# Kernel optimization log

Measured on AMD Instinct MI355X. Metric: run time of the kernel, lower is better.

Reference implementation:

```python
import jax, jax.numpy as jnp
import numpy as np

P = 21            # patch_size
DP = 2            # dilation_patch
PAD = DP * (P // 2)  # 20
EPS = 1e-5


def setup_inputs() -> dict:
    key = jax.random.key(0)
    k1, k2 = jax.random.split(key)
    B, T_total, C, H, W = 4, 8, 64, 64, 64
    out_channels = 64
    feats_ts = jax.random.normal(k1, (B, T_total, C, H, W), dtype=jnp.float32)
    bn_gamma = jnp.ones((P * P,), dtype=jnp.float32)
    bn_beta = jnp.zeros((P * P,), dtype=jnp.float32)
    conv_w = jax.random.normal(k2, (out_channels, P * P), dtype=jnp.float32) * 0.05
    return {"feats_ts": feats_ts, "bn_gamma": bn_gamma, "bn_beta": bn_beta, "conv_w": conv_w}


def _correlation(f1, f2):
    # f1, f2: [N, C, H, W]. SpatialCorrelationSampler with kernel=1, stride=1,
    # pad=0, dilation=1, dilation_patch=2: out[n, p, q, h, w] =
    #   sum_c f1[n, c, h, w] * f2[n, c, h + 2*(p - P//2), w + 2*(q - P//2)]
    N, C, H, W = f1.shape
    padded = jnp.pad(f2, ((0, 0), (0, 0), (PAD, PAD), (PAD, PAD)))
    offs = jnp.arange(P) * DP              # displacement offsets into padded map
    dy = jnp.repeat(offs, P)               # [P*P]
    dx = jnp.tile(offs, P)                 # [P*P]

    def corr_at(oy, ox):
        shifted = jax.lax.dynamic_slice(padded, (0, 0, oy, ox), (N, C, H, W))
        return jnp.einsum('nchw,nchw->nhw', f1, shifted)  # sum over channels

    cor = jax.vmap(corr_at)(dy, dx)        # [P*P, N, H, W]
    return jnp.transpose(cor, (1, 0, 2, 3))  # [N, P*P, H, W]


def reference(feats_ts, bn_gamma, bn_beta, conv_w):
    B, T_total, C, H, W = feats_ts.shape
    T = T_total - 1
    f1 = feats_ts[:, :-1].reshape(B * T, C, H, W)
    f2 = feats_ts[:, 1:].reshape(B * T, C, H, W)

    cor = _correlation(f1, f2)             # [B*T, P*P, H, W]

    # BatchNorm2d (training mode: batch statistics over N, H, W)
    mean = cor.mean(axis=(0, 2, 3))
    var = cor.var(axis=(0, 2, 3))
    xn = (cor - mean[None, :, None, None]) * jax.lax.rsqrt(var + EPS)[None, :, None, None]
    xn = xn * bn_gamma[None, :, None, None] + bn_beta[None, :, None, None]

    # 1x1 conv, no bias: [B*T, out, H, W]
    out = jnp.einsum('nphw,op->nohw', xn, conv_w)
    out = out.reshape(B, T, out.shape[1], H, W)
    # append zero frame along time: [B, T+1, out, H, W]
    out = jnp.concatenate([out, jnp.zeros_like(out[:, :1])], axis=1)
    return out
```

## Files before the change

kernel.cpp:

```cpp
#include <hip/hip_runtime.h>

#define HW   4096
#define CHW  262144
#define NPQ  441
#define KPAD 448
#define CSTR 456
#define CSTA 460

typedef __attribute__((ext_vector_type(8))) short bf16x8;
typedef __attribute__((ext_vector_type(4))) float f32x4;

#define MFMA16(a,b,c) __builtin_amdgcn_mfma_f32_16x16x32_bf16(a,b,c,0,0,0)

__device__ __forceinline__ short f2bf(float f){
  unsigned u = __float_as_uint(f);
  return (short)((u + 0x7FFFu + ((u >> 16) & 1u)) >> 16);
}
__device__ __forceinline__ float bf2f(short s){
  return __uint_as_float(((unsigned)(unsigned short)s) << 16);
}

__device__ __forceinline__ bf16x8 load_fragX(const short* rowX, int pi, int tile,
                                             int kk, int lane){
  const int m = lane & 15, kg = lane >> 4;
  return *(const bf16x8*)(rowX + (2*(tile*16 + m) + pi)*64 + kk*32 + kg*8);
}

__global__ __launch_bounds__(256,4) void k_transpose(const float* __restrict__ feats,
                                                     short* __restrict__ X, int plane0)
{
  __shared__ float tile[64*65];
  const int tid = threadIdx.x;
  const int pll = blockIdx.x >> 6, h = blockIdx.x & 63;
  const float* pb = feats + (size_t)(plane0 + pll)*CHW + h*64;
#pragma unroll
  for (int k = 0; k < 4; ++k){
    const int idx = tid + k*256;
    const int c = idx >> 4, w4 = idx & 15;
    f32x4 v = *(const f32x4*)(pb + c*HW + w4*4);
#pragma unroll
    for (int j = 0; j < 4; ++j) tile[c*65 + w4*4 + j] = v[j];
  }
  __syncthreads();
  short* xb = X + ((size_t)pll*64 + h)*4096;
#pragma unroll
  for (int s = 0; s < 2; ++s){
    const int chunk = tid + s*256;
    const int w = chunk >> 3, cg = chunk & 7;
    bf16x8 r;
#pragma unroll
    for (int j = 0; j < 8; ++j) r[j] = f2bf(tile[(cg*8 + j)*65 + w]);
    *(bf16x8*)(xb + w*64 + cg*8) = r;
  }
}

__global__ __launch_bounds__(256,4) void k_cor2(const short* __restrict__ X,
    short* __restrict__ corg, float* __restrict__ partS, float* __restrict__ partQ)
{
  __shared__ __align__(16) short tile[32*CSTA];
  const int tid = threadIdx.x, wv = tid >> 6, lane = tid & 63;
  const int bi = blockIdx.x;
  const int pi = bi & 1, h = (bi >> 1) & 63, nn = bi >> 7;
  const int pl1 = (nn/7)*8 + (nn%7);
  const short* f1r  = X + ((size_t)pl1*64 + h)*4096;
  const short* f2pl = X + (size_t)(pl1 + 1)*64*4096;

  {
    int4 z = {0,0,0,0};
    for (int idx = tid; idx < 32*CSTA/8; idx += 256) ((int4*)tile)[idx] = z;
  }

  bf16x8 afr[2][2];
#pragma unroll
  for (int mt = 0; mt < 2; ++mt)
#pragma unroll
    for (int kk = 0; kk < 2; ++kk)
      afr[mt][kk] = load_fragX(f1r, pi, mt, kk, lane);

  __syncthreads();

  const int cI = (lane >> 4)*4;
  const int cJ = lane & 15;

  auto clampr = [&](int r){ return r < 0 ? 0 : (r > 63 ? 63 : r); };
  bf16x8 b[4], nb[4];
  {
    const int row0 = clampr(h + 2*wv - 20);
    const short* f2r = f2pl + row0*4096;
    b[0] = load_fragX(f2r, pi, 0, 0, lane);
    b[1] = load_fragX(f2r, pi, 1, 0, lane);
    b[2] = load_fragX(f2r, pi, 0, 1, lane);
    b[3] = load_fragX(f2r, pi, 1, 1, lane);
  }
  for (int it = 0; it < 6; ++it){
    const int u = it*4 + wv;
    const int row = h + 2*u - 20;
    if (it < 5){
      const int rown = clampr(row + 8);
      const short* f2r = f2pl + rown*4096;
      nb[0] = load_fragX(f2r, pi, 0, 0, lane);
      nb[1] = load_fragX(f2r, pi, 1, 0, lane);
      nb[2] = load_fragX(f2r, pi, 0, 1, lane);
      nb[3] = load_fragX(f2r, pi, 1, 1, lane);
    }
    if (u < 21 && (unsigned)row < 64u){
      f32x4 a00 = {0.f,0.f,0.f,0.f}, a01 = a00, a10 = a00, a11 = a00;
      a00 = MFMA16(afr[0][0], b[0], a00);
      a01 = MFMA16(afr[0][0], b[1], a01);
      a10 = MFMA16(afr[1][0], b[0], a10);
      a11 = MFMA16(afr[1][0], b[1], a11);
      a00 = MFMA16(afr[0][1], b[2], a00);
      a01 = MFMA16(afr[0][1], b[3], a01);
      a10 = MFMA16(afr[1][1], b[2], a10);
      a11 = MFMA16(afr[1][1], b[3], a11);
      const int p21 = u*21;
#define SCAT(v, ii, jj) do{ int q_ = (jj) - (ii) + 10; \
        if ((unsigned)q_ < 21u) tile[(ii)*CSTA + p21 + q_] = f2bf(v); }while(0)
#pragma unroll
      for (int r = 0; r < 4; ++r){
        const int i0 = cI + r;
        SCAT(a00[r], i0,      cJ);
        SCAT(a01[r], i0,      cJ + 16);
        SCAT(a10[r], i0 + 16, cJ);
        SCAT(a11[r], i0 + 16, cJ + 16);
      }
#undef SCAT
    }
#pragma unroll
    for (int j = 0; j < 4; ++j) b[j] = nb[j];
  }
  __syncthreads();

  {
    const int g = tid >> 2, sub = tid & 3;
    if (g < 56){
      float s[8], s2[8];
#pragma unroll
      for (int j = 0; j < 8; ++j){ s[j] = 0.f; s2[j] = 0.f; }
      for (int rr = 0; rr < 8; ++rr){
        const int row = sub*8 + rr;
        bf16x8 v = *(const bf16x8*)&tile[row*CSTA + g*8];
#pragma unroll
        for (int j = 0; j < 8; ++j){
          float f = bf2f(v[j]);
          s[j] += f; s2[j] += f*f;
        }
      }
#pragma unroll
      for (int j = 0; j < 8; ++j){
        s[j]  += __shfl_xor(s[j], 1);  s[j]  += __shfl_xor(s[j], 2);
        s2[j] += __shfl_xor(s2[j], 1); s2[j] += __shfl_xor(s2[j], 2);
      }
      if (sub == 0){
        float* ps = partS + (size_t)bi*KPAD + g*8;
        float* pq = partQ + (size_t)bi*KPAD + g*8;
        *(f32x4*)ps       = (f32x4){s[0], s[1], s[2], s[3]};
        *(f32x4*)(ps + 4) = (f32x4){s[4], s[5], s[6], s[7]};
        *(f32x4*)pq       = (f32x4){s2[0], s2[1], s2[2], s2[3]};
        *(f32x4*)(pq + 4) = (f32x4){s2[4], s2[5], s2[6], s2[7]};
      }
    }
  }

  short* cblk = corg + (size_t)bi*14336;
  for (int c = tid; c < 1792; c += 256){
    const int row = c/56, cg = c - row*56;
    *(bf16x8*)(cblk + row*KPAD + cg*8) = *(const bf16x8*)&tile[row*CSTA + cg*8];
  }
}

__global__ __launch_bounds__(256) void k_red2(const float* __restrict__ partS,
    const float* __restrict__ partQ, const float* __restrict__ gamma,
    const float* __restrict__ beta, float* __restrict__ scalek,
    float* __restrict__ shiftk)
{
  __shared__ float redS[4][8], redQ[4][8];
  const int tid = threadIdx.x, wv = tid >> 6, lane = tid & 63;
  const int g = blockIdx.x;
  float s[8], q[8];
#pragma unroll
  for (int j = 0; j < 8; ++j){ s[j] = 0.f; q[j] = 0.f; }
  for (int it = 0; it < 14; ++it){
    const int slot = tid + it*256;
    const float* ps = partS + (size_t)slot*KPAD + g*8;
    const float* pq = partQ + (size_t)slot*KPAD + g*8;
    f32x4 a0 = *(const f32x4*)ps, a1 = *(const f32x4*)(ps + 4);
    f32x4 b0 = *(const f32x4*)pq, b1 = *(const f32x4*)(pq + 4);
#pragma unroll
    for (int j = 0; j < 4; ++j){
      s[j] += a0[j]; s[j+4] += a1[j];
      q[j] += b0[j]; q[j+4] += b1[j];
    }
  }
#pragma unroll
  for (int off = 1; off < 64; off <<= 1){
#pragma unroll
    for (int j = 0; j < 8; ++j){
      s[j] += __shfl_xor(s[j], off);
      q[j] += __shfl_xor(q[j], off);
    }
  }
  if (lane == 0){
#pragma unroll
    for (int j = 0; j < 8; ++j){ redS[wv][j] = s[j]; redQ[wv][j] = q[j]; }
  }
  __syncthreads();
  if (tid < 8){
    const int k = g*8 + tid;
    float st = redS[0][tid] + redS[1][tid] + redS[2][tid] + redS[3][tid];
    float qt = redQ[0][tid] + redQ[1][tid] + redQ[2][tid] + redQ[3][tid];
    float m  = st * (1.f/114688.f);
    float v  = qt * (1.f/114688.f) - m*m;
    float iv = rsqrtf(v + 1e-5f);
    float gm = (k < NPQ) ? gamma[k] : 0.f;
    float bt = (k < NPQ) ? beta[k]  : 0.f;
    float sc = gm * iv;
    scalek[k] = sc;
    shiftk[k] = bt - m*sc;
  }
}

__global__ __launch_bounds__(256) void k_wfold(const float* __restrict__ scalek,
    const float* __restrict__ shiftk, const float* __restrict__ convw,
    short* __restrict__ wpT, float* __restrict__ bias)
{
  __shared__ float red[4];
  const int o = blockIdx.x, tid = threadIdx.x, wv = tid >> 6, lane = tid & 63;
  float part = 0.f;
#pragma unroll
  for (int s = 0; s < 2; ++s){
    const int k = tid + s*256;
    if (k < KPAD){
      float cw = (k < NPQ) ? convw[o*NPQ + k] : 0.f;
      wpT[o*KPAD + k] = f2bf(cw * scalek[k]);
      part += cw * shiftk[k];
    }
  }
#pragma unroll
  for (int off = 1; off < 64; off <<= 1) part += __shfl_xor(part, off);
  if (lane == 0) red[wv] = part;
  __syncthreads();
  if (tid == 0) bias[o] = red[0] + red[1] + red[2] + red[3];
}

__global__ __launch_bounds__(256,2) void k_main2(const short* __restrict__ corg,
    const short* __restrict__ wpT, const float* __restrict__ bias,
    float* __restrict__ out)
{
  __shared__ __align__(16) short cor[64*CSTR];
  const int tid = threadIdx.x, wv = tid >> 6, lane = tid & 63;
  const int nn = blockIdx.x >> 6, h = blockIdx.x & 63;
  const int pl1g = (nn/7)*8 + (nn%7);
  const short* cblk = corg + (size_t)(nn*64 + h)*28672;

#pragma unroll
  for (int s = 0; s < 14; ++s){
    const int c = tid + s*256;
    const int rho = c/56, cg = c - rho*56;
    const int w = ((rho & 31) << 1) | (rho >> 5);
    bf16x8 v = *(const bf16x8*)(cblk + c*8);
    *(bf16x8*)&cor[w*CSTR + cg*8] = v;
  }
  __syncthreads();

  const int m = lane & 15, kg = lane >> 4;
  const short* wrow = wpT + (wv*16 + m)*KPAD;
  f32x4 acc[4];
#pragma unroll
  for (int nt = 0; nt < 4; ++nt) acc[nt] = (f32x4){0.f,0.f,0.f,0.f};
  for (int kk = 0; kk < 14; ++kk){
    const int k0 = kk*32 + kg*8;
    bf16x8 aw = *(const bf16x8*)(wrow + k0);
#pragma unroll
    for (int nt = 0; nt < 4; ++nt){
      bf16x8 bc = *(const bf16x8*)&cor[(nt*16 + m)*CSTR + k0];
      acc[nt] = MFMA16(aw, bc, acc[nt]);
    }
  }
  const int r0 = (lane >> 4)*4;
  float bo[4];
#pragma unroll
  for (int r = 0; r < 4; ++r) bo[r] = bias[wv*16 + r0 + r];
  float* outb = out + (size_t)pl1g*CHW + h*64;
#pragma unroll
  for (int nt = 0; nt < 4; ++nt)
#pragma unroll
    for (int r = 0; r < 4; ++r){
      const int o = wv*16 + r0 + r;
      outb[o*HW + nt*16 + m] = acc[nt][r] + bo[r];
    }
}

__global__ __launch_bounds__(256,4) void k_cor(const short* __restrict__ X,
    short* __restrict__ corg, float* __restrict__ gpartS, float* __restrict__ gpartQ)
{
  __shared__ __align__(16) short tile[32*CSTA];
  const int tid = threadIdx.x, wv = tid >> 6, lane = tid & 63;
  const int bi = blockIdx.x;
  const int pi = bi & 1, h = (bi >> 1) & 63, nn = bi >> 7;
  const int pl1 = (nn/7)*8 + (nn%7);
  const short* f1r  = X + ((size_t)pl1*64 + h)*4096;
  const short* f2pl = X + (size_t)(pl1 + 1)*64*4096;

  {
    int4 z = {0,0,0,0};
    for (int idx = tid; idx < 32*CSTA/8; idx += 256) ((int4*)tile)[idx] = z;
  }
  bf16x8 afr[2][2];
#pragma unroll
  for (int mt = 0; mt < 2; ++mt)
#pragma unroll
    for (int kk = 0; kk < 2; ++kk)
      afr[mt][kk] = load_fragX(f1r, pi, mt, kk, lane);
  __syncthreads();
  const int cI = (lane >> 4)*4;
  const int cJ = lane & 15;
  auto clampr = [&](int r){ return r < 0 ? 0 : (r > 63 ? 63 : r); };
  bf16x8 b[4], nb[4];
  {
    const int row0 = clampr(h + 2*wv - 20);
    const short* f2r = f2pl + row0*4096;
    b[0] = load_fragX(f2r, pi, 0, 0, lane);
    b[1] = load_fragX(f2r, pi, 1, 0, lane);
    b[2] = load_fragX(f2r, pi, 0, 1, lane);
    b[3] = load_fragX(f2r, pi, 1, 1, lane);
  }
  for (int it = 0; it < 6; ++it){
    const int u = it*4 + wv;
    const int row = h + 2*u - 20;
    if (it < 5){
      const int rown = clampr(row + 8);
      const short* f2r = f2pl + rown*4096;
      nb[0] = load_fragX(f2r, pi, 0, 0, lane);
      nb[1] = load_fragX(f2r, pi, 1, 0, lane);
      nb[2] = load_fragX(f2r, pi, 0, 1, lane);
      nb[3] = load_fragX(f2r, pi, 1, 1, lane);
    }
    if (u < 21 && (unsigned)row < 64u){
      f32x4 a00 = {0.f,0.f,0.f,0.f}, a01 = a00, a10 = a00, a11 = a00;
      a00 = MFMA16(afr[0][0], b[0], a00);
      a01 = MFMA16(afr[0][0], b[1], a01);
      a10 = MFMA16(afr[1][0], b[0], a10);
      a11 = MFMA16(afr[1][0], b[1], a11);
      a00 = MFMA16(afr[0][1], b[2], a00);
      a01 = MFMA16(afr[0][1], b[3], a01);
      a10 = MFMA16(afr[1][1], b[2], a10);
      a11 = MFMA16(afr[1][1], b[3], a11);
      const int p21 = u*21;
#define SCAT(v, ii, jj) do{ int q_ = (jj) - (ii) + 10; \
        if ((unsigned)q_ < 21u) tile[(ii)*CSTA + p21 + q_] = f2bf(v); }while(0)
#pragma unroll
      for (int r = 0; r < 4; ++r){
        const int i0 = cI + r;
        SCAT(a00[r], i0,      cJ);
        SCAT(a01[r], i0,      cJ + 16);
        SCAT(a10[r], i0 + 16, cJ);
        SCAT(a11[r], i0 + 16, cJ + 16);
      }
#undef SCAT
    }
#pragma unroll
    for (int j = 0; j < 4; ++j) b[j] = nb[j];
  }
  __syncthreads();
  {
    const int g = tid >> 2, sub = tid & 3;
    if (g < 56){
      float s[8], s2[8];
#pragma unroll
      for (int j = 0; j < 8; ++j){ s[j] = 0.f; s2[j] = 0.f; }
      for (int rr = 0; rr < 8; ++rr){
        const int row = sub*8 + rr;
        bf16x8 v = *(const bf16x8*)&tile[row*CSTA + g*8];
#pragma unroll
        for (int j = 0; j < 8; ++j){
          float f = bf2f(v[j]);
          s[j] += f; s2[j] += f*f;
        }
      }
#pragma unroll
      for (int j = 0; j < 8; ++j){
        s[j]  += __shfl_xor(s[j], 1);  s[j]  += __shfl_xor(s[j], 2);
        s2[j] += __shfl_xor(s2[j], 1); s2[j] += __shfl_xor(s2[j], 2);
      }
      if (sub == 0){
        const int slot = (bi & 31)*KPAD + g*8;
#pragma unroll
        for (int j = 0; j < 8; ++j){
          atomicAdd(&gpartS[slot + j], s[j]);
          atomicAdd(&gpartQ[slot + j], s2[j]);
        }
      }
    }
  }
  short* cblk = corg + (size_t)bi*14336;
  for (int c = tid; c < 1792; c += 256){
    const int row = c/56, cg = c - row*56;
    *(bf16x8*)(cblk + row*KPAD + cg*8) = *(const bf16x8*)&tile[row*CSTA + cg*8];
  }
}

__global__ __launch_bounds__(256) void k_finalizeB(const float* __restrict__ gpartS,
    const float* __restrict__ gpartQ, const float* __restrict__ gamma,
    const float* __restrict__ beta, const float* __restrict__ convw,
    short* __restrict__ wpT, float* __restrict__ bias)
{
  __shared__ float s_scale[NPQ], s_shift[NPQ];
  const int tid = threadIdx.x;
  for (int k = tid; k < NPQ; k += 256){
    float s = 0.f, q = 0.f;
    for (int sl = 0; sl < 32; ++sl){
      s += gpartS[sl*KPAD + k];
      q += gpartQ[sl*KPAD + k];
    }
    float m  = s * (1.f/114688.f);
    float v  = q * (1.f/114688.f) - m*m;
    float iv = rsqrtf(v + 1e-5f);
    float sc = gamma[k] * iv;
    s_scale[k] = sc;
    s_shift[k] = beta[k] - m*sc;
  }
  __syncthreads();
  for (int idx = tid; idx < 64*KPAD; idx += 256){
    int o = idx / KPAD, k = idx - o*KPAD;
    float w = (k < NPQ) ? convw[o*NPQ + k] * s_scale[k] : 0.f;
    wpT[idx] = f2bf(w);
  }
  if (tid < 64){
    float b = 0.f;
    for (int k = 0; k < NPQ; ++k) b += s_shift[k] * convw[tid*NPQ + k];
    bias[tid] = b;
  }
}

__global__ __launch_bounds__(256,2) void k_stats(const short* __restrict__ X,
                                                 float* __restrict__ gsum,
                                                 float* __restrict__ gssq,
                                                 int n0, int plane0)
{
  __shared__ float Gbuf[4*1056];
  __shared__ float s_sum[2][NPQ];
  __shared__ float s_ssq[2][NPQ];
  const int tid = threadIdx.x, wv = tid >> 6, lane = tid & 63;
  const int nn = n0 + (blockIdx.x >> 6), h = blockIdx.x & 63;
  const int pl1 = (nn/7)*8 + (nn%7) - plane0;
  const short* f1r  = X + ((size_t)pl1*64 + h)*4096;
  const short* f2pl = X + (size_t)(pl1 + 1)*64*4096;
  float* Gw = Gbuf + wv*1056;

  for (int i = tid; i < 2*NPQ; i += 256){
    (&s_sum[0][0])[i] = 0.f; (&s_ssq[0][0])[i] = 0.f;
  }
  __syncthreads();

  bf16x8 afr[2][2];
  int cur_pi = -1;
  for (int it = 0; it < 11; ++it){
    const int u = it*4 + wv;
    const bool active = (u < 42);
    const int pi = (u >= 21) ? 1 : 0;
    const int p  = u - pi*21;
    const int row = h + 2*p - 20;
    const bool rv = active && ((unsigned)row < 64u);

    if (active && pi != cur_pi){
#pragma unroll
      for (int mt = 0; mt < 2; ++mt)
#pragma unroll
        for (int kk = 0; kk < 2; ++kk)
          afr[mt][kk] = load_fragX(f1r, pi, mt, kk, lane);
      cur_pi = pi;
    }
    if (rv){
      const short* f2r = f2pl + row*4096;
      f32x4 a00 = {0.f,0.f,0.f,0.f}, a01 = a00, a10 = a00, a11 = a00;
#pragma unroll
      for (int kk = 0; kk < 2; ++kk){
        bf16x8 b0 = load_fragX(f2r, pi, 0, kk, lane);
        bf16x8 b1 = load_fragX(f2r, pi, 1, kk, lane);
        a00 = MFMA16(afr[0][kk], b0, a00);
        a01 = MFMA16(afr[0][kk], b1, a01);
        a10 = MFMA16(afr[1][kk], b0, a10);
        a11 = MFMA16(afr[1][kk], b1, a11);
      }
      const int cI = (lane >> 4)*4;
      const int cJ = lane & 15;
#pragma unroll
      for (int r = 0; r < 4; ++r){
        Gw[(cJ     )*33 + cI + r     ] = a00[r];
        Gw[(cJ + 16)*33 + cI + r     ] = a01[r];
        Gw[(cJ     )*33 + cI + r + 16] = a10[r];
        Gw[(cJ + 16)*33 + cI + r + 16] = a11[r];
      }
    }
    __syncthreads();
    if (rv){
      const int q = lane / 3;
      const int seg = lane - q*3;
      float s = 0.f, s2 = 0.f;
      if (lane < 63){
        const int i0 = seg*11;
        const int i1 = (seg == 2) ? 32 : i0 + 11;
        for (int i = i0; i < i1; ++i){
          const int j = i + q - 10;
          if ((unsigned)j < 32u){
            float v = Gw[j*33 + i];
            s += v; s2 += v*v;
          }
        }
      }
      float sA = __shfl(s,  lane+1), sB = __shfl(s,  lane+2);
      float tA = __shfl(s2, lane+1), tB = __shfl(s2, lane+2);
      if (lane < 63 && seg == 0){
        s_sum[pi][p*21 + q] += s + sA + sB;
        s_ssq[pi][p*21 + q] += s2 + tA + tB;
      }
    }
  }
  __syncthreads();
  for (int i = tid; i < NPQ; i += 256){
    atomicAdd(&gsum[i], s_sum[0][i] + s_sum[1][i]);
    atomicAdd(&gssq[i], s_ssq[0][i] + s_ssq[1][i]);
  }
}

__global__ __launch_bounds__(256) void k_finalizeA(const float* __restrict__ gsum,
    const float* __restrict__ gssq, const float* __restrict__ gamma,
    const float* __restrict__ beta, const float* __restrict__ convw,
    short* __restrict__ wpT, float* __restrict__ bias)
{
  __shared__ float s_scale[NPQ], s_shift[NPQ];
  const int tid = threadIdx.x;
  for (int k = tid; k < NPQ; k += 256){
    float m  = gsum[k] * (1.f/114688.f);
    float v  = gssq[k] * (1.f/114688.f) - m*m;
    float iv = rsqrtf(v + 1e-5f);
    float sc = gamma[k] * iv;
    s_scale[k] = sc;
    s_shift[k] = beta[k] - m*sc;
  }
  __syncthreads();
  for (int idx = tid; idx < 64*KPAD; idx += 256){
    int o = idx / KPAD, k = idx - o*KPAD;
    float w = (k < NPQ) ? convw[o*NPQ + k] * s_scale[k] : 0.f;
    wpT[idx] = f2bf(w);
  }
  if (tid < 64){
    float b = 0.f;
    for (int k = 0; k < NPQ; ++k) b += s_shift[k] * convw[tid*NPQ + k];
    bias[tid] = b;
  }
}

__global__ __launch_bounds__(256,2) void k_main(const short* __restrict__ X,
    const short* __restrict__ wpT, const float* __restrict__ bias,
    float* __restrict__ out, int n0, int plane0)
{
  __shared__ __align__(16) short cor[64*CSTR];
  const int tid = threadIdx.x, wv = tid >> 6, lane = tid & 63;
  const int nn = n0 + (blockIdx.x >> 6), h = blockIdx.x & 63;
  const int pl1g = (nn/7)*8 + (nn%7);
  const int pl1 = pl1g - plane0;
  const short* f1r  = X + ((size_t)pl1*64 + h)*4096;
  const short* f2pl = X + (size_t)(pl1 + 1)*64*4096;

  {
    int4 z = {0,0,0,0};
    for (int idx = tid; idx < 64*CSTR/8; idx += 256) ((int4*)cor)[idx] = z;
  }
  __syncthreads();

  bf16x8 afr[2][2];
  int cur_pi = -1;
  for (int it = 0; it < 11; ++it){
    const int u = it*4 + wv;
    const bool active = (u < 42);
    const int pi = (u >= 21) ? 1 : 0;
    const int p  = u - pi*21;
    const int row = h + 2*p - 20;
    const bool rv = active && ((unsigned)row < 64u);

    if (active && pi != cur_pi){
#pragma unroll
      for (int mt = 0; mt < 2; ++mt)
#pragma unroll
        for (int kk = 0; kk < 2; ++kk)
          afr[mt][kk] = load_fragX(f1r, pi, mt, kk, lane);
      cur_pi = pi;
    }
    if (rv){
      const short* f2r = f2pl + row*4096;
      f32x4 a00 = {0.f,0.f,0.f,0.f}, a01 = a00, a10 = a00, a11 = a00;
#pragma unroll
      for (int kk = 0; kk < 2; ++kk){
        bf16x8 b0 = load_fragX(f2r, pi, 0, kk, lane);
        bf16x8 b1 = load_fragX(f2r, pi, 1, kk, lane);
        a00 = MFMA16(afr[0][kk], b0, a00);
        a01 = MFMA16(afr[0][kk], b1, a01);
        a10 = MFMA16(afr[1][kk], b0, a10);
        a11 = MFMA16(afr[1][kk], b1, a11);
      }
      const int cI = (lane >> 4)*4;
      const int cJ = lane & 15;
      const int p21 = p*21;
#define SCAT(v, ii, jj) do{ int q_ = (jj) - (ii) + 10; \
        if ((unsigned)q_ < 21u) cor[(2*(ii)+pi)*CSTR + p21 + q_] = f2bf(v); }while(0)
#pragma unroll
      for (int r = 0; r < 4; ++r){
        const int i0 = cI + r;
        SCAT(a00[r], i0,      cJ);
        SCAT(a01[r], i0,      cJ + 16);
        SCAT(a10[r], i0 + 16, cJ);
        SCAT(a11[r], i0 + 16, cJ + 16);
      }
#undef SCAT
    }
  }
  __syncthreads();

  const int m = lane & 15, kg = lane >> 4;
  const short* wrow = wpT + (wv*16 + m)*KPAD;
  f32x4 acc[4];
#pragma unroll
  for (int nt = 0; nt < 4; ++nt) acc[nt] = (f32x4){0.f,0.f,0.f,0.f};
  for (int kk = 0; kk < 14; ++kk){
    const int k0 = kk*32 + kg*8;
    bf16x8 aw = *(const bf16x8*)(wrow + k0);
#pragma unroll
    for (int nt = 0; nt < 4; ++nt){
      bf16x8 bc = *(const bf16x8*)&cor[(nt*16 + m)*CSTR + k0];
      acc[nt] = MFMA16(aw, bc, acc[nt]);
    }
  }
  const int r0 = (lane >> 4)*4;
  float bo[4];
#pragma unroll
  for (int r = 0; r < 4; ++r) bo[r] = bias[wv*16 + r0 + r];
  float* outb = out + (size_t)pl1g*CHW + h*64;
#pragma unroll
  for (int nt = 0; nt < 4; ++nt)
#pragma unroll
    for (int r = 0; r < 4; ++r){
      const int o = wv*16 + r0 + r;
      outb[o*HW + nt*16 + m] = acc[nt][r] + bo[r];
    }
}

__global__ __launch_bounds__(256) void k_zero(float* __restrict__ out){
  const int idx = blockIdx.x*256 + threadIdx.x;
  const int b = idx >> 16, r = idx & 65535;
  float4* p = (float4*)(out + (size_t)(b*8 + 7)*CHW);
  p[r] = make_float4(0.f, 0.f, 0.f, 0.f);
}

extern "C" void kernel_launch(void* const* d_in, const int* in_sizes, int n_in,
                              void* d_out, int out_size, void* d_ws, size_t ws_size,
                              hipStream_t stream)
{
  const float* feats = (const float*)d_in[0];
  const float* gamma = (const float*)d_in[1];
  const float* beta  = (const float*)d_in[2];
  const float* convw = (const float*)d_in[3];
  float* out = (float*)d_out;
  float* wsf = (float*)d_ws;

  k_zero<<<1024, 256, 0, stream>>>(out);

  {
    float* scalek = wsf;
    float* shiftk = wsf + 448;
    float* biasB  = wsf + 896;
    short* wpTB   = (short*)(wsf + 1024);
    float* partS  = wsf + 15360;
    float* partQ  = wsf + 1620992;
    short* Xn     = (short*)(wsf + 3226624);
    short* corg   = (short*)(wsf + 7420928);
    const size_t need_p = (size_t)33111040*4;
    if (ws_size >= need_p){
      k_transpose<<<2048, 256, 0, stream>>>(feats, Xn, 0);
      k_cor2<<<3584, 256, 0, stream>>>(Xn, corg, partS, partQ);
      k_red2<<<56, 256, 0, stream>>>(partS, partQ, gamma, beta, scalek, shiftk);
      k_wfold<<<64, 256, 0, stream>>>(scalek, shiftk, convw, wpTB, biasB);
      k_main2<<<1792, 256, 0, stream>>>(corg, wpTB, biasB, out);
      return;
    }
  }

  {
    float* gpartS = wsf;
    float* gpartQ = wsf + 14336;
    float* biasB  = wsf + 28672;
    short* wpTB   = (short*)(wsf + 28736);
    short* Xn     = (short*)(wsf + 43072);
    short* corg   = (short*)(wsf + 4237376);
    const size_t need_a = (size_t)4237376*4 + (size_t)3584*14336*2;
    if (ws_size >= need_a){
      hipMemsetAsync(gpartS, 0, 2*14336*sizeof(float), stream);
      k_transpose<<<2048, 256, 0, stream>>>(feats, Xn, 0);
      k_cor<<<3584, 256, 0, stream>>>(Xn, corg, gpartS, gpartQ);
      k_finalizeB<<<1, 256, 0, stream>>>(gpartS, gpartQ, gamma, beta, convw, wpTB, biasB);
      k_main2<<<1792, 256, 0, stream>>>(corg, wpTB, biasB, out);
      return;
    }
  }

  float* gsum = wsf;
  float* gssq = wsf + 441;
  float* bias = wsf + 896;
  short* wpT  = (short*)(wsf + 1024);
  short* X    = (short*)(wsf + 16384);
  const size_t fixedB = 16384*sizeof(float);
  const size_t planeB = (size_t)CHW*2;

  hipMemsetAsync(gsum, 0, 882*sizeof(float), stream);
  if (ws_size >= fixedB + 32*planeB){
    k_transpose<<<2048, 256, 0, stream>>>(feats, X, 0);
    k_stats<<<1792, 256, 0, stream>>>(X, gsum, gssq, 0, 0);
    k_finalizeA<<<1, 256, 0, stream>>>(gsum, gssq, gamma, beta, convw, wpT, bias);
    k_main<<<1792, 256, 0, stream>>>(X, wpT, bias, out, 0, 0);
  } else if (ws_size >= fixedB + 8*planeB){
    for (int b = 0; b < 4; ++b){
      k_transpose<<<512, 256, 0, stream>>>(feats, X, b*8);
      k_stats<<<448, 256, 0, stream>>>(X, gsum, gssq, b*7, b*8);
    }
    k_finalizeA<<<1, 256, 0, stream>>>(gsum, gssq, gamma, beta, convw, wpT, bias);
    for (int b = 0; b < 4; ++b){
      k_transpose<<<512, 256, 0, stream>>>(feats, X, b*8);
      k_main<<<448, 256, 0, stream>>>(X, wpT, bias, out, b*7, b*8);
    }
  } else {
    for (int n = 0; n < 28; ++n){
      const int pl = (n/7)*8 + (n%7);
      k_transpose<<<128, 256, 0, stream>>>(feats, X, pl);
      k_stats<<<64, 256, 0, stream>>>(X, gsum, gssq, n, pl);
    }
    k_finalizeA<<<1, 256, 0, stream>>>(gsum, gssq, gamma, beta, convw, wpT, bias);
    for (int n = 0; n < 28; ++n){
      const int pl = (n/7)*8 + (n%7);
      k_transpose<<<128, 256, 0, stream>>>(feats, X, pl);
      k_main<<<64, 256, 0, stream>>>(X, wpT, bias, out, n, pl);
    }
  }
}
```

Baseline: 189.8 us.

## Widen correlation blocks to 512 threads and split conv-GEMM into half-row blocks

The correlation kernel now runs 8 waves per block, so each wave handles 3 displacement rows instead of 6. The statistics reduction is re-split across 8 lanes per column group. A new 1x1-conv kernel launches twice as many blocks, each covering half an output row with a smaller LDS tile, and computes the output with bf16 MFMA. The aim is more parallelism and occupancy, at the cost of more blocks, repeated weight loads and less reuse per block.

```diff
diff --git a/kernel.cpp b/kernel.cpp
--- a/kernel.cpp
+++ b/kernel.cpp
@@ -54,7 +54,7 @@
   }
 }
 
-__global__ __launch_bounds__(256,4) void k_cor2(const short* __restrict__ X,
+__global__ __launch_bounds__(512,4) void k_cor3(const short* __restrict__ X,
     short* __restrict__ corg, float* __restrict__ partS, float* __restrict__ partQ)
 {
   __shared__ __align__(16) short tile[32*CSTA];
@@ -67,7 +67,7 @@
 
   {
     int4 z = {0,0,0,0};
-    for (int idx = tid; idx < 32*CSTA/8; idx += 256) ((int4*)tile)[idx] = z;
+    for (int idx = tid; idx < 32*CSTA/8; idx += 512) ((int4*)tile)[idx] = z;
   }
 
   bf16x8 afr[2][2];
@@ -92,11 +92,12 @@
     b[2] = load_fragX(f2r, pi, 0, 1, lane);
     b[3] = load_fragX(f2r, pi, 1, 1, lane);
   }
-  for (int it = 0; it < 6; ++it){
-    const int u = it*4 + wv;
+#pragma unroll
+  for (int it = 0; it < 3; ++it){
+    const int u = it*8 + wv;
     const int row = h + 2*u - 20;
-    if (it < 5){
-      const int rown = clampr(row + 8);
+    if (it < 2){
+      const int rown = clampr(row + 16);
       const short* f2r = f2pl + rown*4096;
       nb[0] = load_fragX(f2r, pi, 0, 0, lane);
       nb[1] = load_fragX(f2r, pi, 1, 0, lane);
@@ -132,13 +133,14 @@
   __syncthreads();
 
   {
-    const int g = tid >> 2, sub = tid & 3;
+    const int g = tid >> 3, sub = tid & 7;
     if (g < 56){
       float s[8], s2[8];
 #pragma unroll
       for (int j = 0; j < 8; ++j){ s[j] = 0.f; s2[j] = 0.f; }
-      for (int rr = 0; rr < 8; ++rr){
-        const int row = sub*8 + rr;
+#pragma unroll
+      for (int rr = 0; rr < 4; ++rr){
+        const int row = sub*4 + rr;
         bf16x8 v = *(const bf16x8*)&tile[row*CSTA + g*8];
 #pragma unroll
         for (int j = 0; j < 8; ++j){
@@ -149,7 +151,9 @@
 #pragma unroll
       for (int j = 0; j < 8; ++j){
         s[j]  += __shfl_xor(s[j], 1);  s[j]  += __shfl_xor(s[j], 2);
+        s[j]  += __shfl_xor(s[j], 4);
         s2[j] += __shfl_xor(s2[j], 1); s2[j] += __shfl_xor(s2[j], 2);
+        s2[j] += __shfl_xor(s2[j], 4);
       }
       if (sub == 0){
         float* ps = partS + (size_t)bi*KPAD + g*8;
@@ -163,7 +167,7 @@
   }
 
   short* cblk = corg + (size_t)bi*14336;
-  for (int c = tid; c < 1792; c += 256){
+  for (int c = tid; c < 1792; c += 512){
     const int row = c/56, cg = c - row*56;
     *(bf16x8*)(cblk + row*KPAD + cg*8) = *(const bf16x8*)&tile[row*CSTA + cg*8];
   }
@@ -241,6 +245,56 @@
   if (lane == 0) red[wv] = part;
   __syncthreads();
   if (tid == 0) bias[o] = red[0] + red[1] + red[2] + red[3];
+}
+
+__global__ __launch_bounds__(256,4) void k_main3(const short* __restrict__ corg,
+    const short* __restrict__ wpT, const float* __restrict__ bias,
+    float* __restrict__ out)
+{
+  __shared__ __align__(16) short cor[32*CSTR];
+  const int tid = threadIdx.x, wv = tid >> 6, lane = tid & 63;
+  const int bi2 = blockIdx.x;
+  const int half = bi2 & 1, h = (bi2 >> 1) & 63, nn = bi2 >> 7;
+  const int pl1g = (nn/7)*8 + (nn%7);
+  const short* cblk = corg + (size_t)(nn*64 + h)*28672;
+
+#pragma unroll
+  for (int s = 0; s < 7; ++s){
+    const int c = tid + s*256;
+    const int rr = c/56, cg = c - rr*56;
+    const int il = rr >> 1, pi = rr & 1;
+    const int grow = pi*32 + half*16 + il;
+    bf16x8 v = *(const bf16x8*)(cblk + grow*KPAD + cg*8);
+    *(bf16x8*)&cor[(2*il + pi)*CSTR + cg*8] = v;
+  }
+  __syncthreads();
+
+  const int m = lane & 15, kg = lane >> 4;
+  const short* wrow = wpT + (wv*16 + m)*KPAD;
+  f32x4 acc[2];
+#pragma unroll
+  for (int nt = 0; nt < 2; ++nt) acc[nt] = (f32x4){0.f,0.f,0.f,0.f};
+  for (int kk = 0; kk < 14; ++kk){
+    const int k0 = kk*32 + kg*8;
+    bf16x8 aw = *(const bf16x8*)(wrow + k0);
+#pragma unroll
+    for (int nt = 0; nt < 2; ++nt){
+      bf16x8 bc = *(const bf16x8*)&cor[(nt*16 + m)*CSTR + k0];
+      acc[nt] = MFMA16(aw, bc, acc[nt]);
+    }
+  }
+  const int r0 = (lane >> 4)*4;
+  float bo[4];
+#pragma unroll
+  for (int r = 0; r < 4; ++r) bo[r] = bias[wv*16 + r0 + r];
+  float* outb = out + (size_t)pl1g*CHW + h*64 + half*32;
+#pragma unroll
+  for (int nt = 0; nt < 2; ++nt)
+#pragma unroll
+    for (int r = 0; r < 4; ++r){
+      const int o = wv*16 + r0 + r;
+      outb[o*HW + nt*16 + m] = acc[nt][r] + bo[r];
+    }
 }
 
 __global__ __launch_bounds__(256,2) void k_main2(const short* __restrict__ corg,
@@ -678,10 +732,10 @@
     const size_t need_p = (size_t)33111040*4;
     if (ws_size >= need_p){
       k_transpose<<<2048, 256, 0, stream>>>(feats, Xn, 0);
-      k_cor2<<<3584, 256, 0, stream>>>(Xn, corg, partS, partQ);
+      k_cor3<<<3584, 512, 0, stream>>>(Xn, corg, partS, partQ);
       k_red2<<<56, 256, 0, stream>>>(partS, partQ, gamma, beta, scalek, shiftk);
       k_wfold<<<64, 256, 0, stream>>>(scalek, shiftk, convw, wpTB, biasB);
-      k_main2<<<1792, 256, 0, stream>>>(corg, wpTB, biasB, out);
+      k_main3<<<3584, 256, 0, stream>>>(corg, wpTB, biasB, out);
       return;
     }
   }
```

Measured after the change: 203.8 us. +7.4%, slower.
